# Kernel tuning notes

Measured on AMD Instinct MI355X. Metric: run time of the kernel, lower is better.

Reference implementation:

```python
import jax, jax.numpy as jnp
import numpy as np

N_NODES = 50000
N_EDGES = 7 * N_NODES  # hex stencil: 6 neighbors + self
BATCH = 4
DIM = 128
N_TYPES = 7


def setup_inputs() -> dict:
    key = jax.random.key(0)
    k_x, k_src, k_dst, k_typ, k_w = jax.random.split(key, 5)
    x = jax.random.normal(k_x, (BATCH, N_NODES, DIM), dtype=jnp.float32)
    src = jax.random.randint(k_src, (N_EDGES,), 0, N_NODES, dtype=jnp.int32)
    dst = jax.random.randint(k_dst, (N_EDGES,), 0, N_NODES, dtype=jnp.int32)
    n_type = jax.random.randint(k_typ, (N_EDGES,), 0, N_TYPES, dtype=jnp.int32)
    edge_index = jnp.stack([src, dst, n_type], axis=0)  # [3, E]
    weight = jax.random.normal(k_w, (1, N_TYPES, DIM), dtype=jnp.float32) * 0.02
    bias = jnp.zeros((1, 1, DIM), dtype=jnp.float32)
    return {"x": x, "edge_index": edge_index, "weight": weight, "bias": bias}


def reference(x, edge_index, weight, bias):
    # x: [B, N, C]; edge_index: [3, E] (src, dst, n_type)
    src, dst, n_type = edge_index[0], edge_index[1], edge_index[2]
    neighbor_features = jnp.take(x, src, axis=1)          # [B, E, C] gather
    w_per_edge = weight[0, n_type, :]                      # [E, C]
    weighted_msgs = neighbor_features * w_per_edge[None]   # [B, E, C] scale
    out = jnp.zeros_like(x).at[:, dst, :].add(weighted_msgs)  # scatter-add over nodes
    return out + bias
```

## Files before the change

### kernel.cpp

```cpp
#include <hip/hip_runtime.h>

#define N_NODES 50000
#define N_EDGES (7 * N_NODES)
#define BATCH 4
#define DIM 128
#define D4 (DIM / 4)
#define CAP 32

#define WS_COUNTS  0
#define WS_OVFCNT  (N_NODES)
#define WS_META    (N_NODES + 48)
#define WS_OVF     (WS_META + N_NODES*CAP)
#define WS_TOTAL_INTS (WS_OVF + 2 * N_EDGES)


__global__ __launch_bounds__(256)
void bucket_scatter_kernel(const int* __restrict__ ei,
                           int* __restrict__ counts,
                           int* __restrict__ ovf_cnt,
                           int* __restrict__ meta,
                           int* __restrict__ ovf) {
    int e = blockIdx.x * 256 + threadIdx.x;
    if (e >= N_EDGES) return;
    int src = ei[e];
    int dst = ei[N_EDGES + e];
    int typ = ei[2 * N_EDGES + e];
    int m = src | (typ << 20);
    int pos = atomicAdd(&counts[dst], 1);
    if (pos < CAP) {
        meta[dst * CAP + pos] = m;
    } else {
        int oi = atomicAdd(ovf_cnt, 1);
        ovf[2 * oi]     = m;
        ovf[2 * oi + 1] = dst;
    }
}

__global__ __launch_bounds__(256)
void gather_kernel(const float* __restrict__ x,
                   const float* __restrict__ w,
                   const float* __restrict__ bias,
                   const int* __restrict__ counts,
                   const int* __restrict__ meta,
                   float* __restrict__ out) {
    int i = blockIdx.x * 256 + threadIdx.x;
    int b = i / (N_NODES * D4);
    int r = i - b * (N_NODES * D4);
    int n  = r >> 5;
    int d4 = r & 31;

    const float4* x4 = reinterpret_cast<const float4*>(x);
    const float4* w4 = reinterpret_cast<const float4*>(w);
    const float4* b4 = reinterpret_cast<const float4*>(bias);

    int cnt = counts[n];
    if (cnt > CAP) cnt = CAP;
    int mreg = meta[n * CAP + d4];

    float4 a = b4[d4];
    for (int k = 0; k < cnt; ++k) {
        int m   = __shfl(mreg, k, 32);
        int src = m & 0xFFFFF;
        int typ = m >> 20;
        float4 wv = w4[typ * D4 + d4];
        float4 xv = x4[(size_t)(b * N_NODES + src) * D4 + d4];
        a.x += wv.x * xv.x;
        a.y += wv.y * xv.y;
        a.z += wv.z * xv.z;
        a.w += wv.w * xv.w;
    }
    reinterpret_cast<float4*>(out)[(size_t)(b * N_NODES + n) * D4 + d4] = a;
}

__global__ __launch_bounds__(256)
void ovf_fix_kernel(const float* __restrict__ x,
                    const float* __restrict__ w,
                    const int* __restrict__ ovf_cnt,
                    const int* __restrict__ ovf,
                    float* __restrict__ out) {
    int total = *ovf_cnt;
    if (total <= 0) return;
    const float4* x4 = reinterpret_cast<const float4*>(x);
    const float4* w4 = reinterpret_cast<const float4*>(w);
    int stride = gridDim.x * blockDim.x;
    for (int t = blockIdx.x * blockDim.x + threadIdx.x; t < total * D4; t += stride) {
        int e  = t >> 5;
        int d4 = t & 31;
        int m   = ovf[2 * e];
        int dst = ovf[2 * e + 1];
        int src = m & 0xFFFFF;
        int typ = m >> 20;
        float4 wv = w4[typ * D4 + d4];
        #pragma unroll
        for (int b = 0; b < BATCH; ++b) {
            float4 xv = x4[(size_t)(b * N_NODES + src) * D4 + d4];
            float* o = out + (size_t)(b * N_NODES + dst) * DIM + d4 * 4;
            atomicAdd(o + 0, wv.x * xv.x);
            atomicAdd(o + 1, wv.y * xv.y);
            atomicAdd(o + 2, wv.z * xv.z);
            atomicAdd(o + 3, wv.w * xv.w);
        }
    }
}


__global__ void init_out_kernel(float* __restrict__ out,
                                const float* __restrict__ bias) {
    int i = blockIdx.x * blockDim.x + threadIdx.x;
    const int total = BATCH * N_NODES * D4;
    if (i >= total) return;
    int d4 = i & (D4 - 1);
    reinterpret_cast<float4*>(out)[i] = reinterpret_cast<const float4*>(bias)[d4];
}

__global__ void edge_scatter_kernel(const float* __restrict__ x,
                                    const int* __restrict__ ei,
                                    const float* __restrict__ w,
                                    float* __restrict__ out) {
    int t = blockIdx.x * blockDim.x + threadIdx.x;
    const int total = N_EDGES * D4;
    if (t >= total) return;
    int e  = t >> 5;
    int d4 = t & 31;
    int src = ei[e];
    int dst = ei[N_EDGES + e];
    int typ = ei[2 * N_EDGES + e];
    const float4* x4 = reinterpret_cast<const float4*>(x);
    float4 wv = reinterpret_cast<const float4*>(w)[typ * D4 + d4];
    #pragma unroll
    for (int b = 0; b < BATCH; ++b) {
        float4 xv = x4[(size_t)(b * N_NODES + src) * D4 + d4];
        float* o = out + (size_t)(b * N_NODES + dst) * DIM + d4 * 4;
        atomicAdd(o + 0, xv.x * wv.x);
        atomicAdd(o + 1, xv.y * wv.y);
        atomicAdd(o + 2, xv.z * wv.z);
        atomicAdd(o + 3, xv.w * wv.w);
    }
}

extern "C" void kernel_launch(void* const* d_in, const int* in_sizes, int n_in,
                              void* d_out, int out_size, void* d_ws, size_t ws_size,
                              hipStream_t stream) {
    const float* x    = (const float*)d_in[0];
    const int*   ei   = (const int*)d_in[1];
    const float* w    = (const float*)d_in[2];
    const float* bias = (const float*)d_in[3];
    float* out = (float*)d_out;

    if (ws_size >= (size_t)WS_TOTAL_INTS * sizeof(int)) {
        int* ws      = (int*)d_ws;
        int* counts  = ws + WS_COUNTS;
        int* ovf_cnt = ws + WS_OVFCNT;
        int* meta    = ws + WS_META;
        int* ovf     = ws + WS_OVF;

        hipMemsetAsync(counts, 0, (N_NODES + 1) * sizeof(int), stream);

        bucket_scatter_kernel<<<(N_EDGES + 255) / 256, 256, 0, stream>>>(
            ei, counts, ovf_cnt, meta, ovf);

        gather_kernel<<<BATCH * N_NODES * D4 / 256, 256, 0, stream>>>(
            x, w, bias, counts, meta, out);

        ovf_fix_kernel<<<64, 256, 0, stream>>>(x, w, ovf_cnt, ovf, out);
    } else {
        init_out_kernel<<<(BATCH * N_NODES * D4 + 255) / 256, 256, 0, stream>>>(out, bias);
        edge_scatter_kernel<<<(N_EDGES * D4 + 255) / 256, 256, 0, stream>>>(x, ei, w, out);
    }
}
```

Before: 277.5 us.

## Process one node per wavefront across batches and pad scatter counters

After: 279.6 us. About the same (+0.8%).

```diff
diff --git a/kernel.cpp b/kernel.cpp
--- a/kernel.cpp
+++ b/kernel.cpp
@@ -6,11 +6,12 @@
 #define DIM 128
 #define D4 (DIM / 4)
 #define CAP 32
+#define CPAD 16
 
 #define WS_COUNTS  0
-#define WS_OVFCNT  (N_NODES)
-#define WS_META    (N_NODES + 48)
-#define WS_OVF     (WS_META + N_NODES*CAP)
+#define WS_OVFCNT  (N_NODES * CPAD)
+#define WS_META    (N_NODES * CPAD + 256)
+#define WS_OVF     (WS_META + N_NODES * CAP)
 #define WS_TOTAL_INTS (WS_OVF + 2 * N_EDGES)
 
 
@@ -26,7 +27,7 @@
     int dst = ei[N_EDGES + e];
     int typ = ei[2 * N_EDGES + e];
     int m = src | (typ << 20);
-    int pos = atomicAdd(&counts[dst], 1);
+    int pos = atomicAdd(&counts[dst * CPAD], 1);
     if (pos < CAP) {
         meta[dst * CAP + pos] = m;
     } else {
@@ -40,36 +41,40 @@
 void gather_kernel(const float* __restrict__ x,
                    const float* __restrict__ w,
                    const float* __restrict__ bias,
-                   const int* __restrict__ counts,
                    const int* __restrict__ meta,
                    float* __restrict__ out) {
-    int i = blockIdx.x * 256 + threadIdx.x;
-    int b = i / (N_NODES * D4);
-    int r = i - b * (N_NODES * D4);
-    int n  = r >> 5;
-    int d4 = r & 31;
+    int lane = threadIdx.x & 63;
+    int d4   = lane & 31;
+    int p    = lane >> 5;
+    int n    = blockIdx.x * 4 + (threadIdx.x >> 6);
+    if (n >= N_NODES) return;
 
     const float4* x4 = reinterpret_cast<const float4*>(x);
     const float4* w4 = reinterpret_cast<const float4*>(w);
     const float4* b4 = reinterpret_cast<const float4*>(bias);
 
-    int cnt = counts[n];
-    if (cnt > CAP) cnt = CAP;
     int mreg = meta[n * CAP + d4];
+    unsigned long long vm = __ballot(mreg != -1);
+    int cnt = __popcll(vm & 0xFFFFFFFFull);
 
-    float4 a = b4[d4];
+    float4 bv = b4[d4];
+    float4 a0 = bv;
+    float4 a1 = bv;
+
     for (int k = 0; k < cnt; ++k) {
-        int m   = __shfl(mreg, k, 32);
+        int m   = __builtin_amdgcn_readlane(mreg, k);
         int src = m & 0xFFFFF;
         int typ = m >> 20;
         float4 wv = w4[typ * D4 + d4];
-        float4 xv = x4[(size_t)(b * N_NODES + src) * D4 + d4];
-        a.x += wv.x * xv.x;
-        a.y += wv.y * xv.y;
-        a.z += wv.z * xv.z;
-        a.w += wv.w * xv.w;
+        float4 v0 = x4[(size_t)(p * N_NODES + src) * D4 + d4];
+        float4 v1 = x4[(size_t)((p + 2) * N_NODES + src) * D4 + d4];
+        a0.x += wv.x * v0.x; a0.y += wv.y * v0.y; a0.z += wv.z * v0.z; a0.w += wv.w * v0.w;
+        a1.x += wv.x * v1.x; a1.y += wv.y * v1.y; a1.z += wv.z * v1.z; a1.w += wv.w * v1.w;
     }
-    reinterpret_cast<float4*>(out)[(size_t)(b * N_NODES + n) * D4 + d4] = a;
+
+    float4* o4 = reinterpret_cast<float4*>(out);
+    o4[(size_t)(p * N_NODES + n) * D4 + d4]       = a0;
+    o4[(size_t)((p + 2) * N_NODES + n) * D4 + d4] = a1;
 }
 
 __global__ __launch_bounds__(256)
@@ -154,13 +159,14 @@
         int* meta    = ws + WS_META;
         int* ovf     = ws + WS_OVF;
 
-        hipMemsetAsync(counts, 0, (N_NODES + 1) * sizeof(int), stream);
+        hipMemsetAsync(counts, 0, (size_t)(N_NODES * CPAD + 1) * sizeof(int), stream);
+        hipMemsetAsync(meta, 0xFF, (size_t)(N_NODES * CAP) * sizeof(int), stream);
 
         bucket_scatter_kernel<<<(N_EDGES + 255) / 256, 256, 0, stream>>>(
             ei, counts, ovf_cnt, meta, ovf);
 
-        gather_kernel<<<BATCH * N_NODES * D4 / 256, 256, 0, stream>>>(
-            x, w, bias, counts, meta, out);
+        gather_kernel<<<(N_NODES + 3) / 4, 256, 0, stream>>>(
+            x, w, bias, meta, out);
 
         ovf_fix_kernel<<<64, 256, 0, stream>>>(x, w, ovf_cnt, ovf, out);
     } else {
```
